# Performance work log

Measured on AMD Instinct MI355X. Metric: run time of the kernel, lower is better.

The kernel has to match this reference:

```python
import jax, jax.numpy as jnp
import numpy as np

EPS = 1e-4


def setup_inputs() -> dict:
    key = jax.random.key(0)
    k1, k2, k3, k4, k5 = jax.random.split(key, 5)
    P, O, H, V = 4096, 32, 26, 48
    point = jax.random.normal(k1, (P, 3), dtype=jnp.float32)
    hyperplane_A = jax.random.normal(k2, (O, H, 3), dtype=jnp.float32)
    hyperplane_b = jax.random.uniform(k3, (O, H), dtype=jnp.float32)
    v1 = jax.random.normal(k4, (O, V, 3), dtype=jnp.float32)
    v2 = jax.random.normal(k5, (O, V, 3), dtype=jnp.float32)
    return {"point": point, "hyperplane_A": hyperplane_A, "hyperplane_b": hyperplane_b, "v1": v1, "v2": v2}


def reference(point, hyperplane_A, hyperplane_b, v1, v2):
    O = hyperplane_A.shape[0]
    pts = point[:, None, None, :]  # (P,1,1,3)

    # --- hyperplane (face) distances ---
    Ap_minus_b = jnp.einsum('pd,ohd->poh', point, hyperplane_A) - hyperplane_b  # (P,O,H)
    Ap_minus_b = jnp.nan_to_num(Ap_minus_b, nan=-jnp.inf, posinf=-jnp.inf)
    is_neg = jnp.all(Ap_minus_b <= 0, axis=-1)  # (P,O) point inside zonotope
    max_vals = jnp.max(Ap_minus_b, axis=-1)
    max_idx = jnp.argmax(Ap_minus_b, axis=-1)

    # project point onto each hyperplane
    pp = pts - Ap_minus_b[..., None] * hyperplane_A  # (P,O,H,3)
    # check projected point against all hyperplanes of the same obstacle
    Appb = jnp.einsum('pohd,ojd->pohj', pp, hyperplane_A) - hyperplane_b[:, None, :]  # (P,O,H,H)
    Appb = jnp.nan_to_num(Appb, nan=-jnp.inf, posinf=-jnp.inf)
    on_zono = jnp.all(Appb <= EPS, axis=-1)  # (P,O,H)

    perp = jnp.linalg.norm(pts - pp, axis=-1)  # (P,O,H)
    perp = jnp.where(on_zono, perp, jnp.inf)
    perp = jnp.nan_to_num(perp, nan=jnp.inf, neginf=jnp.inf)
    min_vals = jnp.min(perp, axis=-1)
    min_idx = jnp.argmin(perp, axis=-1)

    distances = jnp.where(is_neg, max_vals, min_vals)  # (P,O)
    face_idx = jnp.where(is_neg, max_idx, min_idx)     # (P,O)
    gradients = hyperplane_A[jnp.arange(O)[None, :], face_idx]  # (P,O,3)

    # --- edge distances ---
    e = v2 - v1                                         # (O,V,3)
    denom = jnp.sum(e * e, axis=-1, keepdims=True)      # (O,V,1)
    t_hat = jnp.sum((pts - v1) * e, axis=-1, keepdims=True) / denom  # (P,O,V,1)
    t_star = jnp.clip(t_hat, 0.0, 1.0)
    v = v1 + t_star * e                                 # (P,O,V,3)
    edist = jnp.nan_to_num(jnp.linalg.norm(pts - v, axis=-1), nan=jnp.inf)  # (P,O,V)
    e_vals = jnp.min(edist, axis=-1)
    e_idx = jnp.argmin(edist, axis=-1)

    use_edge = (e_vals < distances) & jnp.logical_not(is_neg)  # (P,O)
    idx = jnp.broadcast_to(e_idx[:, :, None, None], e_idx.shape + (1, 3))
    v_sel = jnp.take_along_axis(v, idx, axis=2)[:, :, 0, :]    # (P,O,3)
    safe_d = jnp.where(use_edge, e_vals, 1.0)
    e_grad = (point[:, None, :] - v_sel) / safe_d[..., None]

    distances = jnp.where(use_edge, e_vals, distances)
    gradients = jnp.where(use_edge[..., None], e_grad, gradients)
    return distances, gradients
```

## Files before the change

### kernel.cpp

```cpp
#include <hip/hip_runtime.h>
#include <math.h>

namespace {
constexpr int P = 4096, O = 32, H = 26, V = 48;
constexpr int GPITCH = 28;
constexpr float EPSV = 1e-4f;
}

typedef float f32x2 __attribute__((ext_vector_type(2)));

__device__ __forceinline__ float max3f(float a, float b, float c) {
    return fmaxf(fmaxf(a, b), c);
}
__device__ __forceinline__ unsigned min3u(unsigned a, unsigned b, unsigned c) {
    const unsigned ab = a < b ? a : b;
    return ab < c ? ab : c;
}

__global__ __launch_bounds__(256) void zono_kernel(
    const float* __restrict__ point,
    const float* __restrict__ hA,
    const float* __restrict__ hb,
    const float* __restrict__ v1g,
    const float* __restrict__ v2g,
    float* __restrict__ dist_out,
    float* __restrict__ grad_out)
{
    __shared__ float4 sAb[H];
    __shared__ float  sG[H][GPITCH];
    __shared__ float4 sV1[V];
    __shared__ float4 sE[V];

    const int o   = blockIdx.y;
    const int tid = threadIdx.x;

    if (tid < H) {
        const float* a = hA + (o * H + tid) * 3;
        sAb[tid] = make_float4(a[0], a[1], a[2], hb[o * H + tid]);
    } else if (tid >= 32 && tid < 32 + V) {
        const int v = tid - 32;
        const float* A1 = v1g + (o * V + v) * 3;
        const float* A2 = v2g + (o * V + v) * 3;
        const float x0 = A1[0], x1 = A1[1], x2 = A1[2];
        const float e0 = __fsub_rn(A2[0], x0);
        const float e1 = __fsub_rn(A2[1], x1);
        const float e2 = __fsub_rn(A2[2], x2);
        const float den = __fadd_rn(__fadd_rn(__fmul_rn(e0, e0), __fmul_rn(e1, e1)),
                                    __fmul_rn(e2, e2));
        const float inv = __fdiv_rn(1.f, den);
        const float cv  = __fadd_rn(__fadd_rn(__fmul_rn(x0, e0), __fmul_rn(x1, e1)),
                                    __fmul_rn(x2, e2));
        const float nci = -__fmul_rn(cv, inv);
        sV1[v] = make_float4(x0, x1, x2, inv);
        sE[v]  = make_float4(e0, e1, e2, nci);
    }
    __syncthreads();

    for (int e = tid; e < H * H; e += 256) {
        const int h = e / H;
        const int j = e - h * H;
        const float4 A = sAb[h];
        const float4 B = sAb[j];
        sG[h][j] = __fadd_rn(__fadd_rn(__fmul_rn(A.x, B.x), __fmul_rn(A.y, B.y)),
                             __fmul_rn(A.z, B.z));
    }
    __syncthreads();

    const int p = blockIdx.x * blockDim.x + tid;
    const float p0 = point[p * 3 + 0];
    const float p1 = point[p * 3 + 1];
    const float p2 = point[p * 3 + 2];

    f32x2 s2[13];
    float maxv = -INFINITY; int maxi = 0;
    #pragma unroll
    for (int j = 0; j < H; ++j) {
        const float4 ab = sAb[j];
        const float sj = __fsub_rn(
            __fadd_rn(__fadd_rn(__fmul_rn(p0, ab.x), __fmul_rn(p1, ab.y)),
                      __fmul_rn(p2, ab.z)),
            ab.w);
        s2[j >> 1][j & 1] = sj;
        if (sj > maxv) { maxv = sj; maxi = j; }
    }
    const bool is_neg = (maxv <= 0.f);

    float minpsq = INFINITY; int mini = 0;
    for (int h = 0; h < H; ++h) {
        const float4 ab = sAb[h];
        const float dot = __fadd_rn(__fadd_rn(__fmul_rn(p0, ab.x),
                                              __fmul_rn(p1, ab.y)),
                                    __fmul_rn(p2, ab.z));
        const float nsh = __fsub_rn(ab.w, dot);
        f32x2 nsh2; nsh2.x = nsh; nsh2.y = nsh;

        const f32x2* gRow2 = reinterpret_cast<const f32x2*>(&sG[h][0]);
        f32x2 M0; M0.x = -INFINITY; M0.y = -INFINITY;
        f32x2 M1 = M0;
        #pragma unroll
        for (int q = 0; q < 13; ++q) {
            const f32x2 t = __builtin_elementwise_fma(nsh2, gRow2[q], s2[q]);
            if (q & 1) M1 = __builtin_elementwise_max(M1, t);
            else       M0 = __builtin_elementwise_max(M0, t);
        }
        const f32x2 Mm = __builtin_elementwise_max(M0, M1);
        const bool onz = (fmaxf(Mm.x, Mm.y) < EPSV);

        const float psq = __fmul_rn(__fmul_rn(nsh, nsh), sG[h][h]);
        if (onz && psq < minpsq) { minpsq = psq; mini = h; }
    }
    const float minperp = __fsqrt_rn(minpsq);

    unsigned umin = 0xFFFFFFFFu;
    #pragma unroll 2
    for (int v = 0; v < V; v += 2) {
        unsigned ua, ub;
        {
            const float4 V1 = sV1[v];
            const float4 E  = sE[v];
            const float dpe = __builtin_fmaf(p0, E.x,
                              __builtin_fmaf(p1, E.y, __fmul_rn(p2, E.z)));
            const float th = __builtin_fmaf(dpe, V1.w, E.w);
            const float ts = __builtin_amdgcn_fmed3f(th, 0.f, 1.f);
            const float g0 = __fsub_rn(p0, __builtin_fmaf(ts, E.x, V1.x));
            const float g1 = __fsub_rn(p1, __builtin_fmaf(ts, E.y, V1.y));
            const float g2 = __fsub_rn(p2, __builtin_fmaf(ts, E.z, V1.z));
            const float esq = __builtin_fmaf(g0, g0,
                              __builtin_fmaf(g1, g1, __fmul_rn(g2, g2)));
            ua = (__float_as_uint(esq) & ~63u) | (unsigned)v;
        }
        {
            const float4 V1 = sV1[v + 1];
            const float4 E  = sE[v + 1];
            const float dpe = __builtin_fmaf(p0, E.x,
                              __builtin_fmaf(p1, E.y, __fmul_rn(p2, E.z)));
            const float th = __builtin_fmaf(dpe, V1.w, E.w);
            const float ts = __builtin_amdgcn_fmed3f(th, 0.f, 1.f);
            const float g0 = __fsub_rn(p0, __builtin_fmaf(ts, E.x, V1.x));
            const float g1 = __fsub_rn(p1, __builtin_fmaf(ts, E.y, V1.y));
            const float g2 = __fsub_rn(p2, __builtin_fmaf(ts, E.z, V1.z));
            const float esq = __builtin_fmaf(g0, g0,
                              __builtin_fmaf(g1, g1, __fmul_rn(g2, g2)));
            ub = (__float_as_uint(esq) & ~63u) | (unsigned)(v + 1);
        }
        umin = min3u(ua, ub, umin);
    }
    const int midx = (int)(umin & 63u);

    const float4 V1w = sV1[midx];
    const float4 Ew  = sE[midx];
    const float dpew = __builtin_fmaf(p0, Ew.x,
                       __builtin_fmaf(p1, Ew.y, __fmul_rn(p2, Ew.z)));
    const float thw = __builtin_fmaf(dpew, V1w.w, Ew.w);
    const float tsw = __builtin_amdgcn_fmed3f(thw, 0.f, 1.f);
    const float vm0 = __builtin_fmaf(tsw, Ew.x, V1w.x);
    const float vm1 = __builtin_fmaf(tsw, Ew.y, V1w.y);
    const float vm2 = __builtin_fmaf(tsw, Ew.z, V1w.z);
    const float w0 = __fsub_rn(p0, vm0);
    const float w1 = __fsub_rn(p1, vm1);
    const float w2 = __fsub_rn(p2, vm2);
    const float esqw = __builtin_fmaf(w0, w0,
                       __builtin_fmaf(w1, w1, __fmul_rn(w2, w2)));
    const float mine = __fsqrt_rn(esqw);

    const int   fidx = is_neg ? maxi : mini;
    const float4 ga  = sAb[fidx];
    float dist = is_neg ? maxv : minperp;
    float g0 = ga.x, g1 = ga.y, g2 = ga.z;
    if (!is_neg && (mine < dist)) {
        dist = mine;
        g0 = __fdiv_rn(w0, mine);
        g1 = __fdiv_rn(w1, mine);
        g2 = __fdiv_rn(w2, mine);
    }

    const int idx = p * O + o;
    dist_out[idx] = dist;
    grad_out[idx * 3 + 0] = g0;
    grad_out[idx * 3 + 1] = g1;
    grad_out[idx * 3 + 2] = g2;
}

extern "C" void kernel_launch(void* const* d_in, const int* in_sizes, int n_in,
                              void* d_out, int out_size, void* d_ws, size_t ws_size,
                              hipStream_t stream) {
    const float* point = (const float*)d_in[0];
    const float* hA    = (const float*)d_in[1];
    const float* hb    = (const float*)d_in[2];
    const float* v1    = (const float*)d_in[3];
    const float* v2    = (const float*)d_in[4];
    float* out = (float*)d_out;

    dim3 grid(P / 256, O);
    zono_kernel<<<grid, dim3(256), 0, stream>>>(point, hA, hb, v1, v2,
                                                out, out + P * O);
}
```

Baseline: 17.71 us.

## Split each point's face and edge loops across two lanes with shuffle reduction

Each point is now handled by a pair of adjacent threads. One lane takes faces 0-12 and edges 0-23, the other takes faces 13-25 and edges 24-47, and the two partial minima are merged with xor-shuffles. Block count doubles, so each block now covers 128 points, and only the even lane writes the outputs. This cuts per-thread serial work and raises the number of waves in flight. In exchange, every block still rebuilds the shared Gram matrix and loads its tables, the face-value prologue is computed twice per point, and the closing edge and gradient work is duplicated across both lanes.

```diff
diff --git a/kernel.cpp b/kernel.cpp
--- a/kernel.cpp
+++ b/kernel.cpp
@@ -3,15 +3,13 @@
 
 namespace {
 constexpr int P = 4096, O = 32, H = 26, V = 48;
+constexpr int PPB = 128;
 constexpr int GPITCH = 28;
 constexpr float EPSV = 1e-4f;
 }
 
 typedef float f32x2 __attribute__((ext_vector_type(2)));
 
-__device__ __forceinline__ float max3f(float a, float b, float c) {
-    return fmaxf(fmaxf(a, b), c);
-}
 __device__ __forceinline__ unsigned min3u(unsigned a, unsigned b, unsigned c) {
     const unsigned ab = a < b ? a : b;
     return ab < c ? ab : c;
@@ -66,7 +64,8 @@
     }
     __syncthreads();
 
-    const int p = blockIdx.x * blockDim.x + tid;
+    const int lane = tid & 1;
+    const int p    = blockIdx.x * PPB + (tid >> 1);
     const float p0 = point[p * 3 + 0];
     const float p1 = point[p * 3 + 1];
     const float p2 = point[p * 3 + 2];
@@ -85,8 +84,10 @@
     }
     const bool is_neg = (maxv <= 0.f);
 
-    float minpsq = INFINITY; int mini = 0;
-    for (int h = 0; h < H; ++h) {
+    float minpsq = INFINITY; int mini = lane * 13;
+    const int h0 = lane * 13;
+    for (int k = 0; k < 13; ++k) {
+        const int h = h0 + k;
         const float4 ab = sAb[h];
         const float dot = __fadd_rn(__fadd_rn(__fmul_rn(p0, ab.x),
                                               __fmul_rn(p1, ab.y)),
@@ -109,13 +110,21 @@
         const float psq = __fmul_rn(__fmul_rn(nsh, nsh), sG[h][h]);
         if (onz && psq < minpsq) { minpsq = psq; mini = h; }
     }
+    {
+        const float pv = __shfl_xor(minpsq, 1);
+        const int   pi = __shfl_xor(mini, 1);
+        const bool take = (pv < minpsq) || (pv == minpsq && pi < mini);
+        minpsq = take ? pv : minpsq;  mini = take ? pi : mini;
+    }
     const float minperp = __fsqrt_rn(minpsq);
 
     unsigned umin = 0xFFFFFFFFu;
+    const int v0 = lane * 24;
     #pragma unroll 2
-    for (int v = 0; v < V; v += 2) {
+    for (int vv = 0; vv < 24; vv += 2) {
         unsigned ua, ub;
         {
+            const int v = v0 + vv;
             const float4 V1 = sV1[v];
             const float4 E  = sE[v];
             const float dpe = __builtin_fmaf(p0, E.x,
@@ -130,8 +139,9 @@
             ua = (__float_as_uint(esq) & ~63u) | (unsigned)v;
         }
         {
-            const float4 V1 = sV1[v + 1];
-            const float4 E  = sE[v + 1];
+            const int v = v0 + vv + 1;
+            const float4 V1 = sV1[v];
+            const float4 E  = sE[v];
             const float dpe = __builtin_fmaf(p0, E.x,
                               __builtin_fmaf(p1, E.y, __fmul_rn(p2, E.z)));
             const float th = __builtin_fmaf(dpe, V1.w, E.w);
@@ -141,9 +151,13 @@
             const float g2 = __fsub_rn(p2, __builtin_fmaf(ts, E.z, V1.z));
             const float esq = __builtin_fmaf(g0, g0,
                               __builtin_fmaf(g1, g1, __fmul_rn(g2, g2)));
-            ub = (__float_as_uint(esq) & ~63u) | (unsigned)(v + 1);
+            ub = (__float_as_uint(esq) & ~63u) | (unsigned)v;
         }
         umin = min3u(ua, ub, umin);
+    }
+    {
+        const unsigned pu = (unsigned)__shfl_xor((int)umin, 1);
+        umin = pu < umin ? pu : umin;
     }
     const int midx = (int)(umin & 63u);
 
@@ -174,11 +188,13 @@
         g2 = __fdiv_rn(w2, mine);
     }
 
-    const int idx = p * O + o;
-    dist_out[idx] = dist;
-    grad_out[idx * 3 + 0] = g0;
-    grad_out[idx * 3 + 1] = g1;
-    grad_out[idx * 3 + 2] = g2;
+    if (lane == 0) {
+        const int idx = p * O + o;
+        dist_out[idx] = dist;
+        grad_out[idx * 3 + 0] = g0;
+        grad_out[idx * 3 + 1] = g1;
+        grad_out[idx * 3 + 2] = g2;
+    }
 }
 
 extern "C" void kernel_launch(void* const* d_in, const int* in_sizes, int n_in,
@@ -191,7 +207,7 @@
     const float* v2    = (const float*)d_in[4];
     float* out = (float*)d_out;
 
-    dim3 grid(P / 256, O);
+    dim3 grid(P / PPB, O);
     zono_kernel<<<grid, dim3(256), 0, stream>>>(point, hA, hb, v1, v2,
                                                 out, out + P * O);
 }
```

Measured after the change: 17.12 us. -3.3%, faster.
